# Performance work log

Measured on AMD Instinct MI355X. Metric: run time of the kernel, lower is better.

The kernel has to match this reference:

```python
import jax, jax.numpy as jnp
import numpy as np

B, S, E, H = 2, 2048, 1024, 16
HD = E // H  # head_dim = 64


def setup_inputs() -> dict:
    key = jax.random.key(0)
    k_x, k_wqkv, k_bqkv, k_wo, k_bo = jax.random.split(key, 5)
    # nn.Linear-style init scale ~ 1/sqrt(fan_in)
    s = 1.0 / np.sqrt(E)
    return {
        "x": jax.random.normal(k_x, (B, S, E), dtype=jnp.float32),
        "W_qkv": jax.random.uniform(k_wqkv, (3 * E, E), jnp.float32, -s, s),
        "b_qkv": jax.random.uniform(k_bqkv, (3 * E,), jnp.float32, -s, s),
        "W_out": jax.random.uniform(k_wo, (E, E), jnp.float32, -s, s),
        "b_out": jax.random.uniform(k_bo, (E,), jnp.float32, -s, s),
    }


def reference(x, W_qkv, b_qkv, W_out, b_out):
    # Fused QKV projection: (B,S,E) -> (B,S,3E)
    qkv = jnp.einsum("bse,fe->bsf", x, W_qkv) + b_qkv
    # Faithful to the torch code: reshape to (B,S,H,3*HD), then chunk last dim.
    qkv = qkv.reshape(B, S, H, 3 * HD)
    q, k, v = jnp.split(qkv, 3, axis=-1)  # each (B,S,H,HD)
    scale = 1.0 / jnp.sqrt(jnp.asarray(HD, dtype=x.dtype))
    # scores: (B,H,S,S)
    scores = jnp.einsum("bshd,bthd->bhst", q, k) * scale
    weights = jax.nn.softmax(scores, axis=-1)
    # context: (B,S,H,HD) -> (B,S,E)
    ctx = jnp.einsum("bhst,bthd->bshd", weights, v).reshape(B, S, E)
    return jnp.einsum("bse,fe->bsf", ctx, W_out) + b_out
```

## Files before the change

### kernel.cpp

```cpp
#include <hip/hip_runtime.h>
#include <hip/hip_bf16.h>

#define B_  2
#define S_  2048
#define E_  1024
#define H_  16
#define HD_ 64
#define T_  (B_*S_)
#define F_  (3*E_)

using bf16 = __hip_bfloat16;
typedef __attribute__((ext_vector_type(8))) short bf16x8;
typedef __attribute__((ext_vector_type(4))) short short4v;
typedef __attribute__((ext_vector_type(4))) float f32x4;
typedef __attribute__((ext_vector_type(16))) float f32x16;
typedef __attribute__((ext_vector_type(4))) int i32x4;
typedef __attribute__((ext_vector_type(2))) unsigned int u32x2;

__device__ inline short f2bf(float x) {
  __hip_bfloat16 h = __float2bfloat16(x);
  return __builtin_bit_cast(short, h);
}
__device__ inline float bf2f(short x) {
  return __bfloat162float(__builtin_bit_cast(__hip_bfloat16, x));
}
__device__ inline int pack2(float lo, float hig) {
  return (int)((unsigned short)f2bf(lo) |
               ((unsigned int)(unsigned short)f2bf(hig) << 16));
}

__device__ inline void gload_lds16(const void* g, void* l) {
  __builtin_amdgcn_global_load_lds(
      (const __attribute__((address_space(1))) void*)g,
      (__attribute__((address_space(3))) void*)l, 16, 0, 0);
}

__global__ __launch_bounds__(256) void cvt_f32_bf16(
    const float* __restrict__ in, short* __restrict__ out, int n8) {
  int i = blockIdx.x * 256 + threadIdx.x;
  if (i >= n8) return;
  const float4* p = (const float4*)in + (size_t)i * 2;
  float4 a = p[0], b = p[1];
  bf16x8 r;
  r[0] = f2bf(a.x); r[1] = f2bf(a.y); r[2] = f2bf(a.z); r[3] = f2bf(a.w);
  r[4] = f2bf(b.x); r[5] = f2bf(b.y); r[6] = f2bf(b.z); r[7] = f2bf(b.w);
  *(bf16x8*)(out + (size_t)i * 8) = r;
}

__device__ inline void store_out(short* p, float v) { *p = f2bf(v); }
__device__ inline void store_out(float* p, float v) { *p = v; }

template<typename OutT>
__global__ __launch_bounds__(256) void gemm_nt(
    const short* __restrict__ A,
    const short* __restrict__ Bm,
    const float* __restrict__ bias,
    OutT* __restrict__ C,
    int M, int N, int K) {
  __shared__ __align__(16) char sAB[32768];
  char* sA = sAB;
  char* sB = sAB + 16384;
  const int tid  = threadIdx.x;
  const int w    = tid >> 6, lane = tid & 63;
  const int lr   = lane & 15, g = lane >> 4;
  const int brow = blockIdx.y * 128, bcol = blockIdx.x * 128;
  const int wr   = (w >> 1) * 64,  wc   = (w & 1) * 64;

  f32x4 acc[4][4];
  #pragma unroll
  for (int i = 0; i < 4; ++i)
    #pragma unroll
    for (int j = 0; j < 4; ++j) acc[i][j] = (f32x4)0.0f;

  const size_t Kb = (size_t)K * 2;
  const char* Ag = (const char*)A + (size_t)brow * Kb;
  const char* Bg = (const char*)Bm + (size_t)bcol * Kb;

  for (int k0 = 0; k0 < K; k0 += 64) {
    #pragma unroll
    for (int i = 0; i < 4; ++i) {
      int base = i * 4096 + w * 1024;
      int lb   = base + lane * 16;
      int r    = lb >> 7;
      int cb   = (lb & 127) ^ ((r & 7) << 4);
      gload_lds16(Ag + (size_t)r * Kb + (size_t)k0 * 2 + cb, sA + base);
      gload_lds16(Bg + (size_t)r * Kb + (size_t)k0 * 2 + cb, sB + base);
    }
    __syncthreads();
    #pragma unroll
    for (int ks = 0; ks < 2; ++ks) {
      bf16x8 af[4], bfr[4];
      #pragma unroll
      for (int m = 0; m < 4; ++m) {
        int row = wr + m * 16 + lr;
        int cb  = (ks * 64 + g * 16) ^ ((row & 7) << 4);
        af[m] = *(const bf16x8*)(sA + row * 128 + cb);
      }
      #pragma unroll
      for (int n = 0; n < 4; ++n) {
        int row = wc + n * 16 + lr;
        int cb  = (ks * 64 + g * 16) ^ ((row & 7) << 4);
        bfr[n] = *(const bf16x8*)(sB + row * 128 + cb);
      }
      #pragma unroll
      for (int m = 0; m < 4; ++m)
        #pragma unroll
        for (int n = 0; n < 4; ++n)
          acc[m][n] = __builtin_amdgcn_mfma_f32_16x16x32_bf16(
              af[m], bfr[n], acc[m][n], 0, 0, 0);
    }
    __syncthreads();
  }
  #pragma unroll
  for (int n = 0; n < 4; ++n) {
    int f = bcol + wc + n * 16 + lr;
    float bv = bias[f];
    #pragma unroll
    for (int m = 0; m < 4; ++m) {
      int t0 = brow + wr + m * 16 + g * 4;
      #pragma unroll
      for (int j = 0; j < 4; ++j) {
        store_out(&C[(size_t)(t0 + j) * N + f], acc[m][n][j] + bv);
      }
    }
  }
}

__global__ __launch_bounds__(256) void attn_kernel(
    const short* __restrict__ qkv, short* __restrict__ ctx) {
  __shared__ __align__(16) char smem[16384];
  char* sK  = smem;
  char* sVt = smem + 8192;
  const int tid = threadIdx.x;
  const int w = tid >> 6, lane = tid & 63;
  const int ql = lane & 31, hi = lane >> 5;
  const int qblk = blockIdx.x, h = blockIdx.y, b = blockIdx.z;

  const size_t rowB = (size_t)F_ * 2;
  const char* base = (const char*)qkv + (size_t)b * S_ * rowB + (size_t)h * 384;

  const int qrow = qblk * 128 + w * 32 + ql;
  const char* qp = base + (size_t)qrow * rowB;
  bf16x8 qf[4];
  #pragma unroll
  for (int ks = 0; ks < 4; ++ks) {
    bf16x8 t = *(const bf16x8*)(qp + ks * 32 + hi * 16);
    #pragma unroll
    for (int j = 0; j < 8; ++j) t[j] = f2bf(bf2f(t[j]) * 0.180336880f);
    qf[ks] = t;
  }

  const int vkg = tid >> 4;
  const int vfg = tid & 15;

  float m_run = -3.0e38f, l_run = 0.0f;
  f32x16 ot0 = (f32x16)0.0f, ot1 = (f32x16)0.0f;

  for (int kt = 0; kt < 32; ++kt) {
    const char* kvbase = base + (size_t)(kt * 64) * rowB;
    #pragma unroll
    for (int i = 0; i < 2; ++i) {
      int lbase = i * 4096 + w * 1024;
      int lb = lbase + lane * 16;
      int r  = lb >> 7;
      int cb = (lb & 127) ^ ((r & 7) << 4);
      gload_lds16(kvbase + (size_t)r * rowB + 128 + cb, sK + lbase);
    }
    {
      const char* vp = kvbase + 256 + vfg * 8;
      short4v v0 = *(const short4v*)(vp + (size_t)(vkg * 4 + 0) * rowB);
      short4v v1 = *(const short4v*)(vp + (size_t)(vkg * 4 + 1) * rowB);
      short4v v2 = *(const short4v*)(vp + (size_t)(vkg * 4 + 2) * rowB);
      short4v v3 = *(const short4v*)(vp + (size_t)(vkg * 4 + 3) * rowB);
      #pragma unroll
      for (int f = 0; f < 4; ++f) {
        int fr = vfg * 4 + f;
        u32x2 dw;
        dw[0] = (unsigned short)v0[f] | ((unsigned int)(unsigned short)v1[f] << 16);
        dw[1] = (unsigned short)v2[f] | ((unsigned int)(unsigned short)v3[f] << 16);
        *(u32x2*)(sVt + fr * 128 + ((vkg * 8) ^ ((fr & 7) << 4))) = dw;
      }
    }
    __syncthreads();

    f32x16 st0 = (f32x16)0.0f, st1 = (f32x16)0.0f;
    __builtin_amdgcn_s_setprio(1);
    #pragma unroll
    for (int ks = 0; ks < 4; ++ks) {
      int cb = (ks * 32 + hi * 16) ^ ((ql & 7) << 4);
      bf16x8 k0 = *(const bf16x8*)(sK + ql * 128 + cb);
      bf16x8 k1 = *(const bf16x8*)(sK + (ql + 32) * 128 + cb);
      st0 = __builtin_amdgcn_mfma_f32_32x32x16_bf16(k0, qf[ks], st0, 0, 0, 0);
      st1 = __builtin_amdgcn_mfma_f32_32x32x16_bf16(k1, qf[ks], st1, 0, 0, 0);
    }
    __builtin_amdgcn_s_setprio(0);

    float mx = fmaxf(st0[0], st1[0]);
    #pragma unroll
    for (int r = 1; r < 16; ++r) mx = fmaxf(mx, fmaxf(st0[r], st1[r]));
    mx = fmaxf(mx, __shfl_xor(mx, 32));
    float mn = fmaxf(m_run, mx);
    float al = exp2f(m_run - mn);
    m_run = mn;
    float p0[16], p1[16];
    float rs = 0.0f;
    #pragma unroll
    for (int r = 0; r < 16; ++r) {
      p0[r] = exp2f(st0[r] - mn);
      p1[r] = exp2f(st1[r] - mn);
      rs += p0[r] + p1[r];
    }
    rs += __shfl_xor(rs, 32);
    l_run = l_run * al + rs;
    #pragma unroll
    for (int r = 0; r < 16; ++r) { ot0[r] *= al; ot1[r] *= al; }

    float q0[16], q1[16];
    #pragma unroll
    for (int r = 0; r < 16; ++r) q0[r] = __shfl_xor(p0[r], 32);
    #pragma unroll
    for (int r = 0; r < 16; ++r) q1[r] = __shfl_xor(p1[r], 32);

    i32x4 paw0, paw1, paw2, paw3;
#define BUILD_PAW(dst, pp, qq, bb) do {                                   \
      float v0_ = hi ? qq[(bb)+4] : pp[(bb)+0];                           \
      float v1_ = hi ? qq[(bb)+5] : pp[(bb)+1];                           \
      float v2_ = hi ? qq[(bb)+6] : pp[(bb)+2];                           \
      float v3_ = hi ? qq[(bb)+7] : pp[(bb)+3];                           \
      float v4_ = hi ? pp[(bb)+4] : qq[(bb)+0];                           \
      float v5_ = hi ? pp[(bb)+5] : qq[(bb)+1];                           \
      float v6_ = hi ? pp[(bb)+6] : qq[(bb)+2];                           \
      float v7_ = hi ? pp[(bb)+7] : qq[(bb)+3];                           \
      dst[0] = pack2(v0_, v1_); dst[1] = pack2(v2_, v3_);                 \
      dst[2] = pack2(v4_, v5_); dst[3] = pack2(v6_, v7_); } while (0)
    BUILD_PAW(paw0, p0, q0, 0);
    BUILD_PAW(paw1, p0, q0, 8);
    BUILD_PAW(paw2, p1, q1, 0);
    BUILD_PAW(paw3, p1, q1, 8);
#undef BUILD_PAW

    __builtin_amdgcn_s_setprio(1);
    #pragma unroll
    for (int ks = 0; ks < 4; ++ks) {
      int cb = (ks * 32 + hi * 16) ^ ((ql & 7) << 4);
      bf16x8 pf = __builtin_bit_cast(
          bf16x8, ks == 0 ? paw0 : ks == 1 ? paw1 : ks == 2 ? paw2 : paw3);
      bf16x8 v0 = *(const bf16x8*)(sVt + ql * 128 + cb);
      bf16x8 v1 = *(const bf16x8*)(sVt + (ql + 32) * 128 + cb);
      ot0 = __builtin_amdgcn_mfma_f32_32x32x16_bf16(v0, pf, ot0, 0, 0, 0);
      ot1 = __builtin_amdgcn_mfma_f32_32x32x16_bf16(v1, pf, ot1, 0, 0, 0);
    }
    __builtin_amdgcn_s_setprio(0);
    __syncthreads();
  }

  float inv = 1.0f / l_run;
  short* crow = ctx + ((size_t)b * S_ + qrow) * E_ + h * 64;
  #pragma unroll
  for (int i = 0; i < 8; ++i) {
    int f0 = ((2 * i) & 3) + 8 * (i >> 1) + 4 * hi;
    int w0 = pack2(ot0[2 * i] * inv, ot0[2 * i + 1] * inv);
    int w1 = pack2(ot1[2 * i] * inv, ot1[2 * i + 1] * inv);
    *(int*)(crow + f0)      = w0;
    *(int*)(crow + f0 + 32) = w1;
  }
}

extern "C" void kernel_launch(void* const* d_in, const int* in_sizes, int n_in,
                              void* d_out, int out_size, void* d_ws, size_t ws_size,
                              hipStream_t stream) {
  const float* x    = (const float*)d_in[0];
  const float* Wqkv = (const float*)d_in[1];
  const float* bqkv = (const float*)d_in[2];
  const float* Wout = (const float*)d_in[3];
  const float* bout = (const float*)d_in[4];

  char* ws = (char*)d_ws;
  short* xb    = (short*)(ws);
  short* wqkvb = (short*)(ws + 8388608);
  short* woutb = (short*)(ws + 8388608 + 6291456);
  short* qkvb  = (short*)(ws + 16777216);
  short* ctx   = (short*)(ws + 16777216 + 25165824);

  cvt_f32_bf16<<<2048, 256, 0, stream>>>(x, xb, (T_ * E_) / 8);
  cvt_f32_bf16<<<1536, 256, 0, stream>>>(Wqkv, wqkvb, (F_ * E_) / 8);
  cvt_f32_bf16<<<512, 256, 0, stream>>>(Wout, woutb, (E_ * E_) / 8);

  gemm_nt<short><<<dim3(F_ / 128, T_ / 128), 256, 0, stream>>>(
      xb, wqkvb, bqkv, qkvb, T_, F_, E_);

  attn_kernel<<<dim3(S_ / 128, H_, B_), 256, 0, stream>>>(qkvb, ctx);

  gemm_nt<float><<<dim3(E_ / 128, T_ / 128), 256, 0, stream>>>(
      ctx, woutb, bout, (float*)d_out, T_, E_, E_);
}
```

Before: 255.8 us.

## Double-buffer K/V tiles in attention and add lazy softmax rescaling

The attention kernel now uses two LDS buffers and prefetches the next K tile (async global-to-LDS) and V tile (into registers, transposed into LDS after the PV MFMAs), so global loads overlap compute and one barrier per iteration is dropped. The online softmax skips the rescale of the running max and accumulators unless some lane's max exceeds the running max by more than 8 (log2 units). Probabilities are packed to bf16 before the cross-half shuffles, halving shuffle count. The LDS swizzle gains an extra bit for rows 8-15. LDS doubles to 32KB and register pressure rises, which may reduce occupancy.

Result: faster. 234.0 us (-8.5%).

```diff
diff --git a/kernel.cpp b/kernel.cpp
--- a/kernel.cpp
+++ b/kernel.cpp
@@ -9,6 +9,8 @@
 #define T_  (B_*S_)
 #define F_  (3*E_)
 
+#define SW(r) ((((r) & 7) << 4) ^ (((r) & 8) << 2))
+
 using bf16 = __hip_bfloat16;
 typedef __attribute__((ext_vector_type(8))) short bf16x8;
 typedef __attribute__((ext_vector_type(4))) short short4v;
@@ -24,7 +26,7 @@
 __device__ inline float bf2f(short x) {
   return __bfloat162float(__builtin_bit_cast(__hip_bfloat16, x));
 }
-__device__ inline int pack2(float lo, float hig) {
+__device__ inline int pk2(float lo, float hig) {
   return (int)((unsigned short)f2bf(lo) |
                ((unsigned int)(unsigned short)f2bf(hig) << 16));
 }
@@ -128,9 +130,7 @@
 
 __global__ __launch_bounds__(256) void attn_kernel(
     const short* __restrict__ qkv, short* __restrict__ ctx) {
-  __shared__ __align__(16) char smem[16384];
-  char* sK  = smem;
-  char* sVt = smem + 8192;
+  __shared__ __align__(16) char smem[32768];
   const int tid = threadIdx.x;
   const int w = tid >> 6, lane = tid & 63;
   const int ql = lane & 31, hi = lane >> 5;
@@ -156,38 +156,62 @@
   float m_run = -3.0e38f, l_run = 0.0f;
   f32x16 ot0 = (f32x16)0.0f, ot1 = (f32x16)0.0f;
 
-  for (int kt = 0; kt < 32; ++kt) {
-    const char* kvbase = base + (size_t)(kt * 64) * rowB;
+  {
     #pragma unroll
     for (int i = 0; i < 2; ++i) {
       int lbase = i * 4096 + w * 1024;
       int lb = lbase + lane * 16;
       int r  = lb >> 7;
-      int cb = (lb & 127) ^ ((r & 7) << 4);
-      gload_lds16(kvbase + (size_t)r * rowB + 128 + cb, sK + lbase);
-    }
-    {
-      const char* vp = kvbase + 256 + vfg * 8;
-      short4v v0 = *(const short4v*)(vp + (size_t)(vkg * 4 + 0) * rowB);
-      short4v v1 = *(const short4v*)(vp + (size_t)(vkg * 4 + 1) * rowB);
-      short4v v2 = *(const short4v*)(vp + (size_t)(vkg * 4 + 2) * rowB);
-      short4v v3 = *(const short4v*)(vp + (size_t)(vkg * 4 + 3) * rowB);
-      #pragma unroll
-      for (int f = 0; f < 4; ++f) {
-        int fr = vfg * 4 + f;
-        u32x2 dw;
-        dw[0] = (unsigned short)v0[f] | ((unsigned int)(unsigned short)v1[f] << 16);
-        dw[1] = (unsigned short)v2[f] | ((unsigned int)(unsigned short)v3[f] << 16);
-        *(u32x2*)(sVt + fr * 128 + ((vkg * 8) ^ ((fr & 7) << 4))) = dw;
-      }
-    }
-    __syncthreads();
+      int cb = (lb & 127) ^ SW(r);
+      gload_lds16(base + (size_t)r * rowB + 128 + cb, smem + lbase);
+    }
+    const char* vp = base + 256 + vfg * 8;
+    short4v v0 = *(const short4v*)(vp + (size_t)(vkg * 4 + 0) * rowB);
+    short4v v1 = *(const short4v*)(vp + (size_t)(vkg * 4 + 1) * rowB);
+    short4v v2 = *(const short4v*)(vp + (size_t)(vkg * 4 + 2) * rowB);
+    short4v v3 = *(const short4v*)(vp + (size_t)(vkg * 4 + 3) * rowB);
+    char* dvt = smem + 8192;
+    #pragma unroll
+    for (int f = 0; f < 4; ++f) {
+      int fr = vfg * 4 + f;
+      u32x2 dw;
+      dw[0] = (unsigned short)v0[f] | ((unsigned int)(unsigned short)v1[f] << 16);
+      dw[1] = (unsigned short)v2[f] | ((unsigned int)(unsigned short)v3[f] << 16);
+      *(u32x2*)(dvt + fr * 128 + ((vkg * 8) ^ SW(fr))) = dw;
+    }
+  }
+  __syncthreads();
+
+  int cur = 0;
+  for (int kt = 0; kt < 32; ++kt) {
+    const int nxt = cur ^ 1;
+    const char* sK  = smem + cur * 16384;
+    const char* sVt = sK + 8192;
+
+    short4v nv0, nv1, nv2, nv3;
+    const char* nkvb = base + (size_t)((kt + 1) * 64) * rowB;
+    if (kt < 31) {
+      #pragma unroll
+      for (int i = 0; i < 2; ++i) {
+        int lbase = i * 4096 + w * 1024;
+        int lb = lbase + lane * 16;
+        int r  = lb >> 7;
+        int cb = (lb & 127) ^ SW(r);
+        gload_lds16(nkvb + (size_t)r * rowB + 128 + cb,
+                    smem + nxt * 16384 + lbase);
+      }
+      const char* vp = nkvb + 256 + vfg * 8;
+      nv0 = *(const short4v*)(vp + (size_t)(vkg * 4 + 0) * rowB);
+      nv1 = *(const short4v*)(vp + (size_t)(vkg * 4 + 1) * rowB);
+      nv2 = *(const short4v*)(vp + (size_t)(vkg * 4 + 2) * rowB);
+      nv3 = *(const short4v*)(vp + (size_t)(vkg * 4 + 3) * rowB);
+    }
 
     f32x16 st0 = (f32x16)0.0f, st1 = (f32x16)0.0f;
     __builtin_amdgcn_s_setprio(1);
     #pragma unroll
     for (int ks = 0; ks < 4; ++ks) {
-      int cb = (ks * 32 + hi * 16) ^ ((ql & 7) << 4);
+      int cb = (ks * 32 + hi * 16) ^ SW(ql);
       bf16x8 k0 = *(const bf16x8*)(sK + ql * 128 + cb);
       bf16x8 k1 = *(const bf16x8*)(sK + (ql + 32) * 128 + cb);
       st0 = __builtin_amdgcn_mfma_f32_32x32x16_bf16(k0, qf[ks], st0, 0, 0, 0);
@@ -199,59 +223,71 @@
     #pragma unroll
     for (int r = 1; r < 16; ++r) mx = fmaxf(mx, fmaxf(st0[r], st1[r]));
     mx = fmaxf(mx, __shfl_xor(mx, 32));
-    float mn = fmaxf(m_run, mx);
-    float al = exp2f(m_run - mn);
-    m_run = mn;
+    if (!__all(mx <= m_run + 8.0f)) {
+      float mn = fmaxf(m_run, mx);
+      float al = exp2f(m_run - mn);
+      m_run = mn;
+      l_run *= al;
+      #pragma unroll
+      for (int r = 0; r < 16; ++r) { ot0[r] *= al; ot1[r] *= al; }
+    }
     float p0[16], p1[16];
     float rs = 0.0f;
     #pragma unroll
     for (int r = 0; r < 16; ++r) {
-      p0[r] = exp2f(st0[r] - mn);
-      p1[r] = exp2f(st1[r] - mn);
+      p0[r] = exp2f(st0[r] - m_run);
+      p1[r] = exp2f(st1[r] - m_run);
       rs += p0[r] + p1[r];
     }
     rs += __shfl_xor(rs, 32);
-    l_run = l_run * al + rs;
-    #pragma unroll
-    for (int r = 0; r < 16; ++r) { ot0[r] *= al; ot1[r] *= al; }
-
-    float q0[16], q1[16];
-    #pragma unroll
-    for (int r = 0; r < 16; ++r) q0[r] = __shfl_xor(p0[r], 32);
-    #pragma unroll
-    for (int r = 0; r < 16; ++r) q1[r] = __shfl_xor(p1[r], 32);
-
-    i32x4 paw0, paw1, paw2, paw3;
-#define BUILD_PAW(dst, pp, qq, bb) do {                                   \
-      float v0_ = hi ? qq[(bb)+4] : pp[(bb)+0];                           \
-      float v1_ = hi ? qq[(bb)+5] : pp[(bb)+1];                           \
-      float v2_ = hi ? qq[(bb)+6] : pp[(bb)+2];                           \
-      float v3_ = hi ? qq[(bb)+7] : pp[(bb)+3];                           \
-      float v4_ = hi ? pp[(bb)+4] : qq[(bb)+0];                           \
-      float v5_ = hi ? pp[(bb)+5] : qq[(bb)+1];                           \
-      float v6_ = hi ? pp[(bb)+6] : qq[(bb)+2];                           \
-      float v7_ = hi ? pp[(bb)+7] : qq[(bb)+3];                           \
-      dst[0] = pack2(v0_, v1_); dst[1] = pack2(v2_, v3_);                 \
-      dst[2] = pack2(v4_, v5_); dst[3] = pack2(v6_, v7_); } while (0)
-    BUILD_PAW(paw0, p0, q0, 0);
-    BUILD_PAW(paw1, p0, q0, 8);
-    BUILD_PAW(paw2, p1, q1, 0);
-    BUILD_PAW(paw3, p1, q1, 8);
-#undef BUILD_PAW
+    l_run += rs;
+
+    int pa[8], pb[8], pc[8], pd[8];
+    #pragma unroll
+    for (int r = 0; r < 8; ++r) pa[r] = pk2(p0[2 * r], p0[2 * r + 1]);
+    #pragma unroll
+    for (int r = 0; r < 8; ++r) pb[r] = __shfl_xor(pa[r], 32);
+    #pragma unroll
+    for (int r = 0; r < 8; ++r) pc[r] = pk2(p1[2 * r], p1[2 * r + 1]);
+    #pragma unroll
+    for (int r = 0; r < 8; ++r) pd[r] = __shfl_xor(pc[r], 32);
+    i32x4 paw[4];
+    paw[0][0] = hi ? pb[2] : pa[0];  paw[0][1] = hi ? pb[3] : pa[1];
+    paw[0][2] = hi ? pa[2] : pb[0];  paw[0][3] = hi ? pa[3] : pb[1];
+    paw[1][0] = hi ? pb[6] : pa[4];  paw[1][1] = hi ? pb[7] : pa[5];
+    paw[1][2] = hi ? pa[6] : pb[4];  paw[1][3] = hi ? pa[7] : pb[5];
+    paw[2][0] = hi ? pd[2] : pc[0];  paw[2][1] = hi ? pd[3] : pc[1];
+    paw[2][2] = hi ? pc[2] : pd[0];  paw[2][3] = hi ? pc[3] : pd[1];
+    paw[3][0] = hi ? pd[6] : pc[4];  paw[3][1] = hi ? pd[7] : pc[5];
+    paw[3][2] = hi ? pc[6] : pd[4];  paw[3][3] = hi ? pc[7] : pd[5];
 
     __builtin_amdgcn_s_setprio(1);
     #pragma unroll
     for (int ks = 0; ks < 4; ++ks) {
-      int cb = (ks * 32 + hi * 16) ^ ((ql & 7) << 4);
-      bf16x8 pf = __builtin_bit_cast(
-          bf16x8, ks == 0 ? paw0 : ks == 1 ? paw1 : ks == 2 ? paw2 : paw3);
+      int cb = (ks * 32 + hi * 16) ^ SW(ql);
+      bf16x8 pf = __builtin_bit_cast(bf16x8, paw[ks]);
       bf16x8 v0 = *(const bf16x8*)(sVt + ql * 128 + cb);
       bf16x8 v1 = *(const bf16x8*)(sVt + (ql + 32) * 128 + cb);
       ot0 = __builtin_amdgcn_mfma_f32_32x32x16_bf16(v0, pf, ot0, 0, 0, 0);
       ot1 = __builtin_amdgcn_mfma_f32_32x32x16_bf16(v1, pf, ot1, 0, 0, 0);
     }
     __builtin_amdgcn_s_setprio(0);
+
+    if (kt < 31) {
+      char* dvt = smem + nxt * 16384 + 8192;
+      #pragma unroll
+      for (int f = 0; f < 4; ++f) {
+        int fr = vfg * 4 + f;
+        u32x2 dw;
+        dw[0] = (unsigned short)nv0[f] |
+                ((unsigned int)(unsigned short)nv1[f] << 16);
+        dw[1] = (unsigned short)nv2[f] |
+                ((unsigned int)(unsigned short)nv3[f] << 16);
+        *(u32x2*)(dvt + fr * 128 + ((vkg * 8) ^ SW(fr))) = dw;
+      }
+    }
     __syncthreads();
+    cur = nxt;
   }
 
   float inv = 1.0f / l_run;
@@ -259,8 +295,8 @@
   #pragma unroll
   for (int i = 0; i < 8; ++i) {
     int f0 = ((2 * i) & 3) + 8 * (i >> 1) + 4 * hi;
-    int w0 = pack2(ot0[2 * i] * inv, ot0[2 * i + 1] * inv);
-    int w1 = pack2(ot1[2 * i] * inv, ot1[2 * i + 1] * inv);
+    int w0 = pk2(ot0[2 * i] * inv, ot0[2 * i + 1] * inv);
+    int w1 = pk2(ot1[2 * i] * inv, ot1[2 * i + 1] * inv);
     *(int*)(crow + f0)      = w0;
     *(int*)(crow + f0 + 32) = w1;
   }
```
